# Performance work log

Hardware: AMD Instinct MI355X
Metric: run time of the kernel (lower is better)

## Reference

```python
import jax, jax.numpy as jnp
import numpy as np

N_NODES = 50000
N_EDGES = 1000000
HID = 64
L = 3
EPS_MSG = 1e-7   # GENConv message eps
EPS_SM = 1e-16   # PyG scatter-softmax denominator eps
LN_EPS = 1e-5


def layernorm(x, g, b):
    mu = jnp.mean(x, axis=-1, keepdims=True)
    var = jnp.var(x, axis=-1, keepdims=True)
    return (x - mu) * jax.lax.rsqrt(var + LN_EPS) * g + b


def genconv(x, src, dst, edge_attr, t, W1, b1, g1, be1, W2, b2):
    # message: relu(x_j + e_ij) + eps  -> [E, HID]
    msg = jax.nn.relu(x[src] + edge_attr) + EPS_MSG
    # softmax aggregation over incoming edges of each dst node
    logits = msg * t
    m = jax.ops.segment_max(logits, dst, num_segments=N_NODES)
    m = jnp.where(jnp.isfinite(m), m, 0.0)
    e = jnp.exp(logits - m[dst])
    s = jax.ops.segment_sum(e, dst, num_segments=N_NODES) + EPS_SM
    agg = jax.ops.segment_sum((e / s[dst]) * msg, dst, num_segments=N_NODES)
    # root residual + MLP [64 -> 128 -> 64]
    h = agg + x
    h = h @ W1 + b1
    h = jax.nn.relu(layernorm(h, g1, be1))
    return h @ W2 + b2


def setup_inputs() -> dict:
    key = jax.random.key(0)
    ks = jax.random.split(key, 10)
    inp = {
        'x': jax.random.normal(ks[0], (N_NODES, 16), jnp.float32),
        'edge_attr': jax.random.uniform(ks[1], (N_EDGES, 1), jnp.float32),
        'edge_index': jax.random.randint(ks[2], (2, N_EDGES), 0, N_NODES, jnp.int32),
        'W_node': jax.random.normal(ks[3], (16, HID), jnp.float32) / np.sqrt(16.0),
        'b_node': jnp.zeros((HID,), jnp.float32),
        'W_edge': jax.random.normal(ks[4], (1, HID), jnp.float32),
        'b_edge': jnp.zeros((HID,), jnp.float32),
        't': jnp.ones((L,), jnp.float32),
        'W1': jax.random.normal(ks[5], (L, HID, 2 * HID), jnp.float32) / np.sqrt(float(HID)),
        'b1': jnp.zeros((L, 2 * HID), jnp.float32),
        'ln_g': jnp.ones((L, 2 * HID), jnp.float32),
        'ln_b': jnp.zeros((L, 2 * HID), jnp.float32),
        'W2': jax.random.normal(ks[6], (L, 2 * HID, HID), jnp.float32) / np.sqrt(2.0 * HID),
        'b2': jnp.zeros((L, HID), jnp.float32),
        'norm_g': jnp.ones((L, HID), jnp.float32),
        'norm_b': jnp.zeros((L, HID), jnp.float32),
        'W_lin': jax.random.normal(ks[7], (HID, 64), jnp.float32) / np.sqrt(float(HID)),
        'b_lin': jnp.zeros((64,), jnp.float32),
    }
    return inp


def reference(x, edge_attr, edge_index, W_node, b_node, W_edge, b_edge, t,
              W1, b1, ln_g, ln_b, W2, b2, norm_g, norm_b, W_lin, b_lin):
    src, dst = edge_index[0], edge_index[1]
    h = x @ W_node + b_node                 # [N, HID]
    ea = edge_attr @ W_edge + b_edge        # [E, HID]
    # layer 0: conv only
    h = genconv(h, src, dst, ea, t[0], W1[0], b1[0], ln_g[0], ln_b[0], W2[0], b2[0])
    # layers 1..L-1: res+ blocks (norm -> relu -> conv -> residual); dropout is identity in eval
    for i in range(1, L):
        z = jax.nn.relu(layernorm(h, norm_g[i], norm_b[i]))
        h = h + genconv(z, src, dst, ea, t[i], W1[i], b1[i], ln_g[i], ln_b[i], W2[i], b2[i])
    # final norm/act reuses layer 0's norm
    h = jax.nn.relu(layernorm(h, norm_g[0], norm_b[0]))
    # adaptive avg/max pool (N, 64) -> (1, 32): pool over all nodes, channel bins of 2
    avg = h.mean(axis=0).reshape(32, 2).mean(axis=1)
    mx = h.max(axis=0).reshape(32, 2).max(axis=1)
    emb = jnp.concatenate([avg, mx])[None, :]   # [1, 64]
    return emb @ W_lin + b_lin                  # [1, 64]
```

## Files before the change

### kernel.cpp

```cpp
#include <hip/hip_runtime.h>
#include <math.h>

#define N_NODES 50000
#define N_EDGES 1000000
#define HID 64
#define CAP 64
#define N_TILES (N_NODES / 16)
#define NB_MLP 512
#define VB_S 72
#define UB_S 136
#define NB_ENC ((N_NODES + 3) / 4)
#define NB_WPREP ((3 * 8192 + 255) / 256)
#define NBK 196
#define BKCAP 6144
#define EPB 4096
#define NB1 ((N_EDGES + EPB - 1) / EPB)
static_assert(N_NODES % 16 == 0, "tile math");
static_assert(N_NODES <= 65536, "src must fit in 16 bits");

typedef __attribute__((ext_vector_type(8))) short short8;
typedef __attribute__((ext_vector_type(4))) float f32x4;

__device__ __forceinline__ unsigned short f2bf(float x) {
    unsigned u = __float_as_uint(x);
    u += 0x7FFFu + ((u >> 16) & 1u);
    return (unsigned short)(u >> 16);
}
__device__ __forceinline__ float bfbits_hi(unsigned pk) {
    return __uint_as_float(pk & 0xFFFF0000u);
}
__device__ __forceinline__ float bf2f(unsigned short v) {
    return __uint_as_float(((unsigned)v) << 16);
}
__device__ __forceinline__ unsigned addpk(unsigned a, unsigned b) {
    float lo = __uint_as_float(a << 16) + __uint_as_float(b << 16);
    float hi = __uint_as_float(a & 0xFFFF0000u) + __uint_as_float(b & 0xFFFF0000u);
    return (unsigned)f2bf(lo) | ((unsigned)f2bf(hi) << 16);
}

__global__ __launch_bounds__(256) void k_front(
    const float* __restrict__ x, const float* __restrict__ Wn,
    const float* __restrict__ bn, unsigned short* __restrict__ zb,
    const float* __restrict__ W1, const float* __restrict__ W2,
    unsigned short* __restrict__ w1p, unsigned short* __restrict__ w2p) {
    int b = blockIdx.x;
    if (b < NB_ENC) {
        int n = b * 4 + (threadIdx.x >> 6);
        int c = threadIdx.x & 63;
        if (n >= N_NODES) return;
        float acc = bn[c];
        const float* xr = x + n * 16;
        #pragma unroll
        for (int k = 0; k < 16; ++k) acc = fmaf(xr[k], Wn[k * 64 + c], acc);
        zb[n * 64 + c] = f2bf(acc);
    } else {
        int i = (b - NB_ENC) * 256 + threadIdx.x;
        if (i >= 3 * 8192) return;
        int L = i >> 13, r = i & 8191;
        int j = r & 7, lane = (r >> 3) & 63;
        int quad = lane >> 4, col = lane & 15;
        {
            int st = r >> 9;
            int s = st >> 3, t = st & 7;
            w1p[i] = f2bf(W1[L * 8192 + (s * 32 + quad * 8 + j) * 128 + t * 16 + col]);
        }
        {
            int ft = r >> 9;
            int s = ft >> 2, t = ft & 3;
            w2p[i] = f2bf(W2[L * 8192 + (s * 32 + quad * 8 + j) * 64 + t * 16 + col]);
        }
    }
}

__global__ __launch_bounds__(256) void k_bin1(
    const int* __restrict__ ei, const float* __restrict__ eattr,
    int* __restrict__ gcnt, uint2* __restrict__ coarse) {
    __shared__ unsigned pk_l[EPB];
    __shared__ unsigned short dst_l[EPB];
    __shared__ unsigned spk[EPB];
    __shared__ unsigned short sdst[EPB];
    __shared__ int hist[NBK], loc[NBK], gbase[NBK], cur[NBK];
    __shared__ int inc[256];
    int tid = threadIdx.x;
    int e0 = blockIdx.x * EPB;
    int nel = N_EDGES - e0; if (nel > EPB) nel = EPB;
    for (int b = tid; b < NBK; b += 256) { hist[b] = 0; cur[b] = 0; }
    __syncthreads();
    for (int j = tid; j < nel; j += 256) {
        int i = e0 + j;
        int d = ei[N_EDGES + i];
        unsigned pk = ((unsigned)f2bf(eattr[i]) << 16) | (unsigned)(ei[i] & 0xFFFF);
        pk_l[j] = pk; dst_l[j] = (unsigned short)d;
        atomicAdd(&hist[d >> 8], 1);
    }
    __syncthreads();
    int v = (tid < NBK) ? hist[tid] : 0;
    inc[tid] = v;
    __syncthreads();
    #pragma unroll
    for (int dd = 1; dd < 256; dd <<= 1) {
        int t2 = (tid >= dd) ? inc[tid - dd] : 0;
        __syncthreads();
        inc[tid] += t2;
        __syncthreads();
    }
    if (tid < NBK) {
        loc[tid] = inc[tid] - v;
        gbase[tid] = atomicAdd(&gcnt[tid], v);
    }
    __syncthreads();
    for (int j = tid; j < nel; j += 256) {
        int bkt = dst_l[j] >> 8;
        int r = atomicAdd(&cur[bkt], 1);
        int pos = loc[bkt] + r;
        spk[pos] = pk_l[j]; sdst[pos] = dst_l[j];
    }
    __syncthreads();
    for (int j = tid; j < nel; j += 256) {
        int d = sdst[j];
        int bkt = d >> 8;
        int off = gbase[bkt] + (j - loc[bkt]);
        if (off < BKCAP) coarse[(size_t)bkt * BKCAP + off] = make_uint2(spk[j], (unsigned)d);
    }
}

__global__ __launch_bounds__(256) void k_bin2(
    const int* __restrict__ gcnt, const uint2* __restrict__ coarse,
    int* __restrict__ cnt, unsigned int* __restrict__ s_pack) {
    __shared__ unsigned epk[BKCAP];
    __shared__ unsigned char eln[BKCAP];
    __shared__ unsigned spk[BKCAP];
    __shared__ unsigned char sln[BKCAP];
    __shared__ int hist[256], cur[256], inc2[256];
    int tid = threadIdx.x;
    int b = blockIdx.x;
    int m = gcnt[b]; if (m > BKCAP) m = BKCAP;
    hist[tid] = 0; cur[tid] = 0;
    __syncthreads();
    for (int j = tid; j < m; j += 256) {
        uint2 e = coarse[(size_t)b * BKCAP + j];
        epk[j] = e.x;
        int ln = (int)(e.y & 255u);
        eln[j] = (unsigned char)ln;
        atomicAdd(&hist[ln], 1);
    }
    __syncthreads();
    int v = hist[tid];
    inc2[tid] = v;
    __syncthreads();
    #pragma unroll
    for (int dd = 1; dd < 256; dd <<= 1) {
        int t2 = (tid >= dd) ? inc2[tid - dd] : 0;
        __syncthreads();
        inc2[tid] += t2;
        __syncthreads();
    }
    int lv = inc2[tid] - v;
    __syncthreads();
    hist[tid] = lv;
    int node = b * 256 + tid;
    if (node < N_NODES) cnt[node] = v;
    __syncthreads();
    for (int j = tid; j < m; j += 256) {
        int ln = eln[j];
        int r = atomicAdd(&cur[ln], 1);
        int pos = hist[ln] + r;
        spk[pos] = epk[j]; sln[pos] = (unsigned char)ln;
    }
    __syncthreads();
    for (int j = tid; j < m; j += 256) {
        int ln = sln[j];
        int k = j - hist[ln];
        if (k < CAP) s_pack[(size_t)(b * 256 + ln) * CAP + k] = spk[j];
    }
}

__global__ __launch_bounds__(256) void k_agg(
    const unsigned short* __restrict__ zb, const int* __restrict__ cnt,
    const unsigned int* __restrict__ s_pack,
    const float* __restrict__ We, const float* __restrict__ be,
    const float* __restrict__ t, int layer, unsigned short* __restrict__ aggb) {
    int wid = (blockIdx.x * blockDim.x + threadIdx.x) >> 6;
    int lane = threadIdx.x & 63;
    if (wid >= N_NODES) return;
    int deg = cnt[wid];
    deg = (deg < CAP) ? deg : CAP;
    int beg = wid * CAP, end = beg + deg;
    int half = lane >> 5;
    int c2 = lane & 31;
    float we0 = We[2 * c2], we1 = We[2 * c2 + 1];
    float bv0 = be[2 * c2], bv1 = be[2 * c2 + 1];
    float tl = t[layer];
    const unsigned* zbu = (const unsigned*)zb;
    float s0 = 0.f, s1 = 0.f, n0 = 0.f, n1 = 0.f;
    int i = beg;
    for (; i + 7 < end; i += 8) {
        unsigned pk[4];
        #pragma unroll
        for (int j = 0; j < 4; ++j) {
            unsigned pa = s_pack[i + 2 * j];
            unsigned pb = s_pack[i + 2 * j + 1];
            pk[j] = half ? pb : pa;
        }
        unsigned zu[4];
        #pragma unroll
        for (int j = 0; j < 4; ++j) zu[j] = zbu[(pk[j] & 0xFFFFu) * 32 + c2];
        #pragma unroll
        for (int j = 0; j < 4; ++j) {
            float ea = bfbits_hi(pk[j]);
            float z0 = __uint_as_float(zu[j] << 16);
            float z1 = __uint_as_float(zu[j] & 0xFFFF0000u);
            float m0 = fmaxf(z0 + fmaf(ea, we0, bv0), 0.f) + 1e-7f;
            float m1 = fmaxf(z1 + fmaf(ea, we1, bv1), 0.f) + 1e-7f;
            float p0 = __expf(m0 * tl), p1 = __expf(m1 * tl);
            s0 += p0; n0 = fmaf(p0, m0, n0);
            s1 += p1; n1 = fmaf(p1, m1, n1);
        }
    }
    for (; i + 1 < end; i += 2) {
        unsigned pa = s_pack[i], pb = s_pack[i + 1];
        unsigned pk = half ? pb : pa;
        unsigned zu = zbu[(pk & 0xFFFFu) * 32 + c2];
        float ea = bfbits_hi(pk);
        float z0 = __uint_as_float(zu << 16);
        float z1 = __uint_as_float(zu & 0xFFFF0000u);
        float m0 = fmaxf(z0 + fmaf(ea, we0, bv0), 0.f) + 1e-7f;
        float m1 = fmaxf(z1 + fmaf(ea, we1, bv1), 0.f) + 1e-7f;
        float p0 = __expf(m0 * tl), p1 = __expf(m1 * tl);
        s0 += p0; n0 = fmaf(p0, m0, n0);
        s1 += p1; n1 = fmaf(p1, m1, n1);
    }
    if (i < end) {
        unsigned pk = s_pack[i];
        unsigned zu = zbu[(pk & 0xFFFFu) * 32 + c2];
        float ea = bfbits_hi(pk);
        float z0 = __uint_as_float(zu << 16);
        float z1 = __uint_as_float(zu & 0xFFFF0000u);
        float m0 = fmaxf(z0 + fmaf(ea, we0, bv0), 0.f) + 1e-7f;
        float m1 = fmaxf(z1 + fmaf(ea, we1, bv1), 0.f) + 1e-7f;
        float p0 = __expf(m0 * tl), p1 = __expf(m1 * tl);
        if (half == 0) {
            s0 += p0; n0 = fmaf(p0, m0, n0);
            s1 += p1; n1 = fmaf(p1, m1, n1);
        }
    }
    s0 += __shfl_xor(s0, 32, 64); n0 += __shfl_xor(n0, 32, 64);
    s1 += __shfl_xor(s1, 32, 64); n1 += __shfl_xor(n1, 32, 64);
    if (half == 0) {
        unsigned r = (unsigned)f2bf(n0 / (s0 + 1e-16f)) |
                     ((unsigned)f2bf(n1 / (s1 + 1e-16f)) << 16);
        ((unsigned*)aggb)[wid * 32 + c2] = r;
    }
}

__global__ __launch_bounds__(256) void k_mlp(
    const unsigned short* __restrict__ aggb, unsigned short* __restrict__ zb,
    unsigned short* __restrict__ hb,
    const unsigned short* __restrict__ w1p, const unsigned short* __restrict__ w2p,
    const float* __restrict__ b1,
    const float* __restrict__ g1, const float* __restrict__ be1,
    const float* __restrict__ b2,
    const float* __restrict__ ng, const float* __restrict__ nb, int mode,
    float* __restrict__ pb_sum, float* __restrict__ pb_max) {
    __shared__ unsigned short w1s[8192];
    __shared__ unsigned short w2s[8192];
    __shared__ unsigned short vbuf[4][16 * VB_S];
    __shared__ unsigned short ubuf[4][16 * UB_S];
    __shared__ float lssum[4][4][16], lsmax[4][4][16];
    int lane = threadIdx.x & 63;
    int wave = threadIdx.x >> 6;
    int col = lane & 15, quad = lane >> 4;
    unsigned short* vb = vbuf[wave];
    unsigned short* ub = ubuf[wave];

    {
        const uint4* s1 = (const uint4*)w1p;
        const uint4* s2 = (const uint4*)w2p;
        uint4* d1 = (uint4*)w1s;
        uint4* d2 = (uint4*)w2s;
        #pragma unroll
        for (int i = 0; i < 4; ++i) {
            d1[threadIdx.x + i * 256] = s1[threadIdx.x + i * 256];
            d2[threadIdx.x + i * 256] = s2[threadIdx.x + i * 256];
        }
    }
    __syncthreads();

    float b1f[8], g1f[8], e1f[8];
    #pragma unroll
    for (int t = 0; t < 8; ++t) {
        int ch = t * 16 + col;
        b1f[t] = b1[ch]; g1f[t] = g1[ch]; e1f[t] = be1[ch];
    }
    float b2f_[4], ngf[4], nbf[4];
    #pragma unroll
    for (int t = 0; t < 4; ++t) {
        b2f_[t] = b2[t * 16 + col];
        ngf[t] = ng[t * 16 + col];
        nbf[t] = nb[t * 16 + col];
    }

    float psum[4] = {0.f, 0.f, 0.f, 0.f};
    float pmax[4] = {0.f, 0.f, 0.f, 0.f};
    int nd = lane >> 2;
    int cg = (lane & 3) * 16;

    for (int tile = blockIdx.x * 4 + wave; tile < N_TILES; tile += NB_MLP * 4) {
        int n0 = tile * 16;
        const uint4* ap = (const uint4*)(aggb + (size_t)(n0 + nd) * 64 + cg);
        const uint4* zp = (const uint4*)(zb + (size_t)(n0 + nd) * 64 + cg);
        uint4 a0 = ap[0], a1 = ap[1], z0 = zp[0], z1 = zp[1];
        uint4 r0, r1;
        r0.x = addpk(a0.x, z0.x); r0.y = addpk(a0.y, z0.y);
        r0.z = addpk(a0.z, z0.z); r0.w = addpk(a0.w, z0.w);
        r1.x = addpk(a1.x, z1.x); r1.y = addpk(a1.y, z1.y);
        r1.z = addpk(a1.z, z1.z); r1.w = addpk(a1.w, z1.w);
        uint4* vdst = (uint4*)&vb[nd * VB_S + cg];
        vdst[0] = r0;
        vdst[1] = r1;

        short8 af0 = *(const short8*)&vb[col * VB_S + quad * 8];
        short8 af1 = *(const short8*)&vb[col * VB_S + 32 + quad * 8];

        uint4 h0, h1;
        if (mode >= 1) {
            const uint4* hp = (const uint4*)(hb + (size_t)(n0 + nd) * 64 + cg);
            h0 = hp[0]; h1 = hp[1];
        }

        f32x4 au[8];
        #pragma unroll
        for (int t = 0; t < 8; ++t) {
            short8 w0 = *(const short8*)&w1s[((0 * 8 + t) * 64 + lane) * 8];
            short8 w1 = *(const short8*)&w1s[((1 * 8 + t) * 64 + lane) * 8];
            f32x4 c = {0.f, 0.f, 0.f, 0.f};
            c = __builtin_amdgcn_mfma_f32_16x16x32_bf16(af0, w0, c, 0, 0, 0);
            c = __builtin_amdgcn_mfma_f32_16x16x32_bf16(af1, w1, c, 0, 0, 0);
            au[t] = c;
        }
        #pragma unroll
        for (int r = 0; r < 4; ++r) {
            float sx = 0.f, sq = 0.f;
            #pragma unroll
            for (int t = 0; t < 8; ++t) {
                float v = au[t][r] + b1f[t];
                sx += v; sq += v * v;
            }
            #pragma unroll
            for (int mask = 1; mask < 16; mask <<= 1) {
                sx += __shfl_xor(sx, mask, 64);
                sq += __shfl_xor(sq, mask, 64);
            }
            float mu = sx * (1.f / 128.f);
            float var = sq * (1.f / 128.f) - mu * mu;
            float rs = rsqrtf(var + 1e-5f);
            int row = quad * 4 + r;
            #pragma unroll
            for (int t = 0; t < 8; ++t) {
                float v = au[t][r] + b1f[t];
                float y = fmaxf(fmaf((v - mu) * rs, g1f[t], e1f[t]), 0.f);
                ub[row * UB_S + t * 16 + col] = f2bf(y);
            }
        }
        f32x4 oc[4];
        #pragma unroll
        for (int t = 0; t < 4; ++t) oc[t] = (f32x4){0.f, 0.f, 0.f, 0.f};
        #pragma unroll
        for (int s = 0; s < 4; ++s) {
            short8 a = *(const short8*)&ub[col * UB_S + s * 32 + quad * 8];
            #pragma unroll
            for (int t = 0; t < 4; ++t) {
                short8 w = *(const short8*)&w2s[((s * 4 + t) * 64 + lane) * 8];
                oc[t] = __builtin_amdgcn_mfma_f32_16x16x32_bf16(a, w, oc[t], 0, 0, 0);
            }
        }
        if (mode >= 1) {
            uint4* hdst = (uint4*)&vb[nd * VB_S + cg];
            hdst[0] = h0;
            hdst[1] = h1;
        }
        #pragma unroll
        for (int r = 0; r < 4; ++r) {
            int row = quad * 4 + r;
            float val[4];
            #pragma unroll
            for (int t = 0; t < 4; ++t) {
                val[t] = oc[t][r] + b2f_[t];
                if (mode >= 1) val[t] += bf2f(vb[row * VB_S + t * 16 + col]);
            }
            float sx = 0.f, sq = 0.f;
            #pragma unroll
            for (int t = 0; t < 4; ++t) { sx += val[t]; sq += val[t] * val[t]; }
            #pragma unroll
            for (int mask = 1; mask < 16; mask <<= 1) {
                sx += __shfl_xor(sx, mask, 64);
                sq += __shfl_xor(sq, mask, 64);
            }
            float mu = sx * (1.f / 64.f);
            float var = sq * (1.f / 64.f) - mu * mu;
            float rs = rsqrtf(var + 1e-5f);
            #pragma unroll
            for (int t = 0; t < 4; ++t) {
                float y = fmaxf(fmaf((val[t] - mu) * rs, ngf[t], nbf[t]), 0.f);
                if (mode <= 1) {
                    vb[row * VB_S + t * 16 + col] = f2bf(val[t]);
                    ub[row * UB_S + t * 16 + col] = f2bf(y);
                } else {
                    psum[t] += y;
                    pmax[t] = fmaxf(pmax[t], y);
                }
            }
        }
        if (mode <= 1) {
            const uint4* hsrc = (const uint4*)&vb[nd * VB_S + cg];
            const uint4* zsrc = (const uint4*)&ub[nd * UB_S + cg];
            uint4* hdst = (uint4*)(hb + (size_t)(n0 + nd) * 64 + cg);
            uint4* zdst = (uint4*)(zb + (size_t)(n0 + nd) * 64 + cg);
            hdst[0] = hsrc[0]; hdst[1] = hsrc[1];
            zdst[0] = zsrc[0]; zdst[1] = zsrc[1];
        }
    }
    if (mode == 2) {
        #pragma unroll
        for (int t = 0; t < 4; ++t) {
            psum[t] += __shfl_xor(psum[t], 16, 64);
            psum[t] += __shfl_xor(psum[t], 32, 64);
            pmax[t] = fmaxf(pmax[t], __shfl_xor(pmax[t], 16, 64));
            pmax[t] = fmaxf(pmax[t], __shfl_xor(pmax[t], 32, 64));
        }
        if (quad == 0) {
            #pragma unroll
            for (int t = 0; t < 4; ++t) {
                lssum[wave][t][col] = psum[t];
                lsmax[wave][t][col] = pmax[t];
            }
        }
        __syncthreads();
        if (wave == 0) {
            int t = lane >> 4, c = lane & 15;
            float s = lssum[0][t][c] + lssum[1][t][c] + lssum[2][t][c] + lssum[3][t][c];
            float mx = fmaxf(fmaxf(lsmax[0][t][c], lsmax[1][t][c]),
                             fmaxf(lsmax[2][t][c], lsmax[3][t][c]));
            pb_sum[blockIdx.x * 64 + lane] = s;
            pb_max[blockIdx.x * 64 + lane] = mx;
        }
    }
}

__global__ __launch_bounds__(1024) void k_head(
    const float* __restrict__ pb_sum, const float* __restrict__ pb_max,
    const float* __restrict__ Wl, const float* __restrict__ bl, float* __restrict__ out) {
    __shared__ float sa4[16][64], sm4[16][64];
    __shared__ float sa[64], sm[64], emb[64];
    int t = threadIdx.x;
    int ch = t & 63, part = t >> 6;
    float s = 0.f, mx = 0.f;
    for (int b = part; b < NB_MLP; b += 16) {
        s += pb_sum[b * 64 + ch];
        mx = fmaxf(mx, pb_max[b * 64 + ch]);
    }
    sa4[part][ch] = s; sm4[part][ch] = mx;
    __syncthreads();
    if (t < 64) {
        float ss = 0.f, mm = 0.f;
        #pragma unroll
        for (int q = 0; q < 16; ++q) {
            ss += sa4[q][t];
            mm = fmaxf(mm, sm4[q][t]);
        }
        sa[t] = ss; sm[t] = mm;
    }
    __syncthreads();
    if (t < 64) {
        if (t < 32) {
            emb[t] = (sa[2 * t] + sa[2 * t + 1]) * (0.5f / (float)N_NODES);
        } else {
            int i = t - 32;
            emb[t] = fmaxf(sm[2 * i], sm[2 * i + 1]);
        }
    }
    __syncthreads();
    if (t < 64) {
        float acc = bl[t];
        for (int k = 0; k < 64; ++k) acc = fmaf(emb[k], Wl[k * 64 + t], acc);
        out[t] = acc;
    }
}

extern "C" void kernel_launch(void* const* d_in, const int* in_sizes, int n_in,
                              void* d_out, int out_size, void* d_ws, size_t ws_size,
                              hipStream_t stream) {
    const float* x     = (const float*)d_in[0];
    const float* eattr = (const float*)d_in[1];
    const int*   ei    = (const int*)d_in[2];
    const float* Wn    = (const float*)d_in[3];
    const float* bn    = (const float*)d_in[4];
    const float* We    = (const float*)d_in[5];
    const float* be    = (const float*)d_in[6];
    const float* t     = (const float*)d_in[7];
    const float* W1    = (const float*)d_in[8];
    const float* b1    = (const float*)d_in[9];
    const float* lg    = (const float*)d_in[10];
    const float* lb    = (const float*)d_in[11];
    const float* W2    = (const float*)d_in[12];
    const float* b2    = (const float*)d_in[13];
    const float* ng    = (const float*)d_in[14];
    const float* nb    = (const float*)d_in[15];
    const float* Wl    = (const float*)d_in[16];
    const float* bl    = (const float*)d_in[17];
    float* out = (float*)d_out;

    char* p = (char*)d_ws;
    unsigned short* hb   = (unsigned short*)p; p += (size_t)N_NODES * 64 * 2;
    unsigned short* zb   = (unsigned short*)p; p += (size_t)N_NODES * 64 * 2;
    unsigned short* aggb = (unsigned short*)p; p += (size_t)N_NODES * 64 * 2;
    unsigned int* s_pack = (unsigned int*)p; p += (size_t)N_NODES * CAP * 4;
    int* cnt    = (int*)p;  p += (size_t)N_NODES * 4;
    int* gcnt   = (int*)p;  p += (size_t)256 * 4;
    uint2* coarse = (uint2*)p; p += (size_t)NBK * BKCAP * 8;
    float* pb_sum = (float*)p; p += (size_t)NB_MLP * 64 * 4;
    float* pb_max = (float*)p; p += (size_t)NB_MLP * 64 * 4;
    unsigned short* w1p = (unsigned short*)p; p += (size_t)3 * 8192 * 2;
    unsigned short* w2p = (unsigned short*)p; p += (size_t)3 * 8192 * 2;

    hipMemsetAsync(gcnt, 0, (size_t)NBK * sizeof(int), stream);

    k_front<<<NB_ENC + NB_WPREP, 256, 0, stream>>>(x, Wn, bn, zb, W1, W2, w1p, w2p);
    k_bin1<<<NB1, 256, 0, stream>>>(ei, eattr, gcnt, coarse);
    k_bin2<<<NBK, 256, 0, stream>>>(gcnt, coarse, cnt, s_pack);

    k_agg<<<(N_NODES + 3) / 4, 256, 0, stream>>>(zb, cnt, s_pack, We, be, t, 0, aggb);
    k_mlp<<<NB_MLP, 256, 0, stream>>>(aggb, zb, hb, w1p, w2p, b1, lg, lb, b2,
                                      ng + 64, nb + 64, 0, pb_sum, pb_max);
    k_agg<<<(N_NODES + 3) / 4, 256, 0, stream>>>(zb, cnt, s_pack, We, be, t, 1, aggb);
    k_mlp<<<NB_MLP, 256, 0, stream>>>(aggb, zb, hb, w1p + 8192, w2p + 8192,
                                      b1 + 128, lg + 128, lb + 128, b2 + 64,
                                      ng + 128, nb + 128, 1, pb_sum, pb_max);
    k_agg<<<(N_NODES + 3) / 4, 256, 0, stream>>>(zb, cnt, s_pack, We, be, t, 2, aggb);
    k_mlp<<<NB_MLP, 256, 0, stream>>>(aggb, zb, hb, w1p + 2 * 8192, w2p + 2 * 8192,
                                      b1 + 2 * 128, lg + 2 * 128, lb + 2 * 128, b2 + 2 * 64,
                                      ng, nb, 2, pb_sum, pb_max);

    k_head<<<1, 1024, 0, stream>>>(pb_sum, pb_max, Wl, bl, out);
}
```

Before: 297.5 us.

## Fuse aggregation into per-tile MLP kernel and merge binning into front kernel

Removes the separate aggregation kernel: each wave now aggregates its 16-node tile in registers and feeds the MFMA MLP directly, using ping-pong z buffers instead of an agg buffer. The first binning pass is folded into the front kernel, and the second pass is split into two half-bucket blocks for more parallelism. Weights are read from global memory rather than staged in LDS, and the grid is sized to one tile per wave. This cuts launches and the agg buffer round trip, but aggregation parallelism drops from one wave per node to one wave per 16 nodes, and the per-tile gather latency is serialized.

Measured after the change: 475.9 us. +60.0%, slower.

```diff
diff --git a/kernel.cpp b/kernel.cpp
--- a/kernel.cpp
+++ b/kernel.cpp
@@ -6,7 +6,7 @@
 #define HID 64
 #define CAP 64
 #define N_TILES (N_NODES / 16)
-#define NB_MLP 512
+#define NB_MLP 782
 #define VB_S 72
 #define UB_S 136
 #define NB_ENC ((N_NODES + 3) / 4)
@@ -42,10 +42,60 @@
     const float* __restrict__ x, const float* __restrict__ Wn,
     const float* __restrict__ bn, unsigned short* __restrict__ zb,
     const float* __restrict__ W1, const float* __restrict__ W2,
-    unsigned short* __restrict__ w1p, unsigned short* __restrict__ w2p) {
+    unsigned short* __restrict__ w1p, unsigned short* __restrict__ w2p,
+    const int* __restrict__ ei, const float* __restrict__ eattr,
+    int* __restrict__ gcnt, uint2* __restrict__ coarse) {
+    __shared__ unsigned pk_l[EPB];
+    __shared__ unsigned short dst_l[EPB];
+    __shared__ unsigned spk[EPB];
+    __shared__ unsigned short sdst[EPB];
+    __shared__ int hist[NBK], loc[NBK], gbase[NBK], cur[NBK];
+    __shared__ int inc[256];
     int b = blockIdx.x;
-    if (b < NB_ENC) {
-        int n = b * 4 + (threadIdx.x >> 6);
+    if (b < NB1) {
+        int tid = threadIdx.x;
+        int e0 = b * EPB;
+        int nel = N_EDGES - e0; if (nel > EPB) nel = EPB;
+        for (int q = tid; q < NBK; q += 256) { hist[q] = 0; cur[q] = 0; }
+        __syncthreads();
+        for (int j = tid; j < nel; j += 256) {
+            int i = e0 + j;
+            int d = ei[N_EDGES + i];
+            unsigned pk = ((unsigned)f2bf(eattr[i]) << 16) | (unsigned)(ei[i] & 0xFFFF);
+            pk_l[j] = pk; dst_l[j] = (unsigned short)d;
+            atomicAdd(&hist[d >> 8], 1);
+        }
+        __syncthreads();
+        int v = (tid < NBK) ? hist[tid] : 0;
+        inc[tid] = v;
+        __syncthreads();
+        #pragma unroll
+        for (int dd = 1; dd < 256; dd <<= 1) {
+            int t2 = (tid >= dd) ? inc[tid - dd] : 0;
+            __syncthreads();
+            inc[tid] += t2;
+            __syncthreads();
+        }
+        if (tid < NBK) {
+            loc[tid] = inc[tid] - v;
+            gbase[tid] = atomicAdd(&gcnt[tid], v);
+        }
+        __syncthreads();
+        for (int j = tid; j < nel; j += 256) {
+            int bkt = dst_l[j] >> 8;
+            int r = atomicAdd(&cur[bkt], 1);
+            int pos = loc[bkt] + r;
+            spk[pos] = pk_l[j]; sdst[pos] = dst_l[j];
+        }
+        __syncthreads();
+        for (int j = tid; j < nel; j += 256) {
+            int d = sdst[j];
+            int bkt = d >> 8;
+            int off = gbase[bkt] + (j - loc[bkt]);
+            if (off < BKCAP) coarse[(size_t)bkt * BKCAP + off] = make_uint2(spk[j], (unsigned)d);
+        }
+    } else if (b < NB1 + NB_ENC) {
+        int n = (b - NB1) * 4 + (threadIdx.x >> 6);
         int c = threadIdx.x & 63;
         if (n >= N_NODES) return;
         float acc = bn[c];
@@ -54,7 +104,7 @@
         for (int k = 0; k < 16; ++k) acc = fmaf(xr[k], Wn[k * 64 + c], acc);
         zb[n * 64 + c] = f2bf(acc);
     } else {
-        int i = (b - NB_ENC) * 256 + threadIdx.x;
+        int i = (b - NB1 - NB_ENC) * 256 + threadIdx.x;
         if (i >= 3 * 8192) return;
         int L = i >> 13, r = i & 8191;
         int j = r & 7, lane = (r >> 3) & 63;
@@ -72,58 +122,6 @@
     }
 }
 
-__global__ __launch_bounds__(256) void k_bin1(
-    const int* __restrict__ ei, const float* __restrict__ eattr,
-    int* __restrict__ gcnt, uint2* __restrict__ coarse) {
-    __shared__ unsigned pk_l[EPB];
-    __shared__ unsigned short dst_l[EPB];
-    __shared__ unsigned spk[EPB];
-    __shared__ unsigned short sdst[EPB];
-    __shared__ int hist[NBK], loc[NBK], gbase[NBK], cur[NBK];
-    __shared__ int inc[256];
-    int tid = threadIdx.x;
-    int e0 = blockIdx.x * EPB;
-    int nel = N_EDGES - e0; if (nel > EPB) nel = EPB;
-    for (int b = tid; b < NBK; b += 256) { hist[b] = 0; cur[b] = 0; }
-    __syncthreads();
-    for (int j = tid; j < nel; j += 256) {
-        int i = e0 + j;
-        int d = ei[N_EDGES + i];
-        unsigned pk = ((unsigned)f2bf(eattr[i]) << 16) | (unsigned)(ei[i] & 0xFFFF);
-        pk_l[j] = pk; dst_l[j] = (unsigned short)d;
-        atomicAdd(&hist[d >> 8], 1);
-    }
-    __syncthreads();
-    int v = (tid < NBK) ? hist[tid] : 0;
-    inc[tid] = v;
-    __syncthreads();
-    #pragma unroll
-    for (int dd = 1; dd < 256; dd <<= 1) {
-        int t2 = (tid >= dd) ? inc[tid - dd] : 0;
-        __syncthreads();
-        inc[tid] += t2;
-        __syncthreads();
-    }
-    if (tid < NBK) {
-        loc[tid] = inc[tid] - v;
-        gbase[tid] = atomicAdd(&gcnt[tid], v);
-    }
-    __syncthreads();
-    for (int j = tid; j < nel; j += 256) {
-        int bkt = dst_l[j] >> 8;
-        int r = atomicAdd(&cur[bkt], 1);
-        int pos = loc[bkt] + r;
-        spk[pos] = pk_l[j]; sdst[pos] = dst_l[j];
-    }
-    __syncthreads();
-    for (int j = tid; j < nel; j += 256) {
-        int d = sdst[j];
-        int bkt = d >> 8;
-        int off = gbase[bkt] + (j - loc[bkt]);
-        if (off < BKCAP) coarse[(size_t)bkt * BKCAP + off] = make_uint2(spk[j], (unsigned)d);
-    }
-}
-
 __global__ __launch_bounds__(256) void k_bin2(
     const int* __restrict__ gcnt, const uint2* __restrict__ coarse,
     int* __restrict__ cnt, unsigned int* __restrict__ s_pack) {
@@ -131,139 +129,66 @@
     __shared__ unsigned char eln[BKCAP];
     __shared__ unsigned spk[BKCAP];
     __shared__ unsigned char sln[BKCAP];
-    __shared__ int hist[256], cur[256], inc2[256];
+    __shared__ int hist[128], loc[128], cur[128], inc2[128];
     int tid = threadIdx.x;
-    int b = blockIdx.x;
-    int m = gcnt[b]; if (m > BKCAP) m = BKCAP;
-    hist[tid] = 0; cur[tid] = 0;
+    int bkt = blockIdx.x >> 1;
+    int hsel = blockIdx.x & 1;
+    int m = gcnt[bkt]; if (m > BKCAP) m = BKCAP;
+    if (tid < 128) { hist[tid] = 0; cur[tid] = 0; }
     __syncthreads();
     for (int j = tid; j < m; j += 256) {
-        uint2 e = coarse[(size_t)b * BKCAP + j];
+        uint2 e = coarse[(size_t)bkt * BKCAP + j];
         epk[j] = e.x;
         int ln = (int)(e.y & 255u);
         eln[j] = (unsigned char)ln;
-        atomicAdd(&hist[ln], 1);
-    }
-    __syncthreads();
-    int v = hist[tid];
-    inc2[tid] = v;
+        if ((ln >> 7) == hsel) atomicAdd(&hist[ln & 127], 1);
+    }
+    __syncthreads();
+    int v = (tid < 128) ? hist[tid] : 0;
+    if (tid < 128) inc2[tid] = v;
     __syncthreads();
     #pragma unroll
-    for (int dd = 1; dd < 256; dd <<= 1) {
-        int t2 = (tid >= dd) ? inc2[tid - dd] : 0;
-        __syncthreads();
-        inc2[tid] += t2;
-        __syncthreads();
-    }
-    int lv = inc2[tid] - v;
-    __syncthreads();
-    hist[tid] = lv;
-    int node = b * 256 + tid;
-    if (node < N_NODES) cnt[node] = v;
-    __syncthreads();
+    for (int dd = 1; dd < 128; dd <<= 1) {
+        int t2 = (tid >= dd && tid < 128) ? inc2[tid - dd] : 0;
+        __syncthreads();
+        if (tid < 128) inc2[tid] += t2;
+        __syncthreads();
+    }
+    if (tid < 128) {
+        loc[tid] = inc2[tid] - v;
+        int node = bkt * 256 + hsel * 128 + tid;
+        if (node < N_NODES) cnt[node] = v;
+    }
+    __syncthreads();
+    int mh = inc2[127];
     for (int j = tid; j < m; j += 256) {
         int ln = eln[j];
-        int r = atomicAdd(&cur[ln], 1);
-        int pos = hist[ln] + r;
-        spk[pos] = epk[j]; sln[pos] = (unsigned char)ln;
-    }
-    __syncthreads();
-    for (int j = tid; j < m; j += 256) {
+        if ((ln >> 7) == hsel) {
+            int r = atomicAdd(&cur[ln & 127], 1);
+            int pos = loc[ln & 127] + r;
+            spk[pos] = epk[j]; sln[pos] = (unsigned char)ln;
+        }
+    }
+    __syncthreads();
+    for (int j = tid; j < mh; j += 256) {
         int ln = sln[j];
-        int k = j - hist[ln];
-        if (k < CAP) s_pack[(size_t)(b * 256 + ln) * CAP + k] = spk[j];
-    }
-}
-
-__global__ __launch_bounds__(256) void k_agg(
-    const unsigned short* __restrict__ zb, const int* __restrict__ cnt,
-    const unsigned int* __restrict__ s_pack,
+        int k = j - loc[ln & 127];
+        if (k < CAP) s_pack[(size_t)(bkt * 256 + ln) * CAP + k] = spk[j];
+    }
+}
+
+__global__ __launch_bounds__(256) void k_layer(
+    const unsigned short* __restrict__ zin, unsigned short* __restrict__ zout,
+    unsigned short* __restrict__ hb,
+    const int* __restrict__ cnt, const unsigned int* __restrict__ s_pack,
     const float* __restrict__ We, const float* __restrict__ be,
-    const float* __restrict__ t, int layer, unsigned short* __restrict__ aggb) {
-    int wid = (blockIdx.x * blockDim.x + threadIdx.x) >> 6;
-    int lane = threadIdx.x & 63;
-    if (wid >= N_NODES) return;
-    int deg = cnt[wid];
-    deg = (deg < CAP) ? deg : CAP;
-    int beg = wid * CAP, end = beg + deg;
-    int half = lane >> 5;
-    int c2 = lane & 31;
-    float we0 = We[2 * c2], we1 = We[2 * c2 + 1];
-    float bv0 = be[2 * c2], bv1 = be[2 * c2 + 1];
-    float tl = t[layer];
-    const unsigned* zbu = (const unsigned*)zb;
-    float s0 = 0.f, s1 = 0.f, n0 = 0.f, n1 = 0.f;
-    int i = beg;
-    for (; i + 7 < end; i += 8) {
-        unsigned pk[4];
-        #pragma unroll
-        for (int j = 0; j < 4; ++j) {
-            unsigned pa = s_pack[i + 2 * j];
-            unsigned pb = s_pack[i + 2 * j + 1];
-            pk[j] = half ? pb : pa;
-        }
-        unsigned zu[4];
-        #pragma unroll
-        for (int j = 0; j < 4; ++j) zu[j] = zbu[(pk[j] & 0xFFFFu) * 32 + c2];
-        #pragma unroll
-        for (int j = 0; j < 4; ++j) {
-            float ea = bfbits_hi(pk[j]);
-            float z0 = __uint_as_float(zu[j] << 16);
-            float z1 = __uint_as_float(zu[j] & 0xFFFF0000u);
-            float m0 = fmaxf(z0 + fmaf(ea, we0, bv0), 0.f) + 1e-7f;
-            float m1 = fmaxf(z1 + fmaf(ea, we1, bv1), 0.f) + 1e-7f;
-            float p0 = __expf(m0 * tl), p1 = __expf(m1 * tl);
-            s0 += p0; n0 = fmaf(p0, m0, n0);
-            s1 += p1; n1 = fmaf(p1, m1, n1);
-        }
-    }
-    for (; i + 1 < end; i += 2) {
-        unsigned pa = s_pack[i], pb = s_pack[i + 1];
-        unsigned pk = half ? pb : pa;
-        unsigned zu = zbu[(pk & 0xFFFFu) * 32 + c2];
-        float ea = bfbits_hi(pk);
-        float z0 = __uint_as_float(zu << 16);
-        float z1 = __uint_as_float(zu & 0xFFFF0000u);
-        float m0 = fmaxf(z0 + fmaf(ea, we0, bv0), 0.f) + 1e-7f;
-        float m1 = fmaxf(z1 + fmaf(ea, we1, bv1), 0.f) + 1e-7f;
-        float p0 = __expf(m0 * tl), p1 = __expf(m1 * tl);
-        s0 += p0; n0 = fmaf(p0, m0, n0);
-        s1 += p1; n1 = fmaf(p1, m1, n1);
-    }
-    if (i < end) {
-        unsigned pk = s_pack[i];
-        unsigned zu = zbu[(pk & 0xFFFFu) * 32 + c2];
-        float ea = bfbits_hi(pk);
-        float z0 = __uint_as_float(zu << 16);
-        float z1 = __uint_as_float(zu & 0xFFFF0000u);
-        float m0 = fmaxf(z0 + fmaf(ea, we0, bv0), 0.f) + 1e-7f;
-        float m1 = fmaxf(z1 + fmaf(ea, we1, bv1), 0.f) + 1e-7f;
-        float p0 = __expf(m0 * tl), p1 = __expf(m1 * tl);
-        if (half == 0) {
-            s0 += p0; n0 = fmaf(p0, m0, n0);
-            s1 += p1; n1 = fmaf(p1, m1, n1);
-        }
-    }
-    s0 += __shfl_xor(s0, 32, 64); n0 += __shfl_xor(n0, 32, 64);
-    s1 += __shfl_xor(s1, 32, 64); n1 += __shfl_xor(n1, 32, 64);
-    if (half == 0) {
-        unsigned r = (unsigned)f2bf(n0 / (s0 + 1e-16f)) |
-                     ((unsigned)f2bf(n1 / (s1 + 1e-16f)) << 16);
-        ((unsigned*)aggb)[wid * 32 + c2] = r;
-    }
-}
-
-__global__ __launch_bounds__(256) void k_mlp(
-    const unsigned short* __restrict__ aggb, unsigned short* __restrict__ zb,
-    unsigned short* __restrict__ hb,
+    const float* __restrict__ t, int layer,
     const unsigned short* __restrict__ w1p, const unsigned short* __restrict__ w2p,
     const float* __restrict__ b1,
     const float* __restrict__ g1, const float* __restrict__ be1,
     const float* __restrict__ b2,
     const float* __restrict__ ng, const float* __restrict__ nb, int mode,
     float* __restrict__ pb_sum, float* __restrict__ pb_max) {
-    __shared__ unsigned short w1s[8192];
-    __shared__ unsigned short w2s[8192];
     __shared__ unsigned short vbuf[4][16 * VB_S];
     __shared__ unsigned short ubuf[4][16 * UB_S];
     __shared__ float lssum[4][4][16], lsmax[4][4][16];
@@ -272,53 +197,99 @@
     int col = lane & 15, quad = lane >> 4;
     unsigned short* vb = vbuf[wave];
     unsigned short* ub = ubuf[wave];
-
-    {
-        const uint4* s1 = (const uint4*)w1p;
-        const uint4* s2 = (const uint4*)w2p;
-        uint4* d1 = (uint4*)w1s;
-        uint4* d2 = (uint4*)w2s;
-        #pragma unroll
-        for (int i = 0; i < 4; ++i) {
-            d1[threadIdx.x + i * 256] = s1[threadIdx.x + i * 256];
-            d2[threadIdx.x + i * 256] = s2[threadIdx.x + i * 256];
-        }
-    }
-    __syncthreads();
-
-    float b1f[8], g1f[8], e1f[8];
-    #pragma unroll
-    for (int t = 0; t < 8; ++t) {
-        int ch = t * 16 + col;
-        b1f[t] = b1[ch]; g1f[t] = g1[ch]; e1f[t] = be1[ch];
-    }
-    float b2f_[4], ngf[4], nbf[4];
-    #pragma unroll
-    for (int t = 0; t < 4; ++t) {
-        b2f_[t] = b2[t * 16 + col];
-        ngf[t] = ng[t * 16 + col];
-        nbf[t] = nb[t * 16 + col];
-    }
-
+    int tile = blockIdx.x * 4 + wave;
     float psum[4] = {0.f, 0.f, 0.f, 0.f};
     float pmax[4] = {0.f, 0.f, 0.f, 0.f};
-    int nd = lane >> 2;
-    int cg = (lane & 3) * 16;
-
-    for (int tile = blockIdx.x * 4 + wave; tile < N_TILES; tile += NB_MLP * 4) {
+
+    if (tile < N_TILES) {
         int n0 = tile * 16;
-        const uint4* ap = (const uint4*)(aggb + (size_t)(n0 + nd) * 64 + cg);
-        const uint4* zp = (const uint4*)(zb + (size_t)(n0 + nd) * 64 + cg);
-        uint4 a0 = ap[0], a1 = ap[1], z0 = zp[0], z1 = zp[1];
-        uint4 r0, r1;
-        r0.x = addpk(a0.x, z0.x); r0.y = addpk(a0.y, z0.y);
-        r0.z = addpk(a0.z, z0.z); r0.w = addpk(a0.w, z0.w);
-        r1.x = addpk(a1.x, z1.x); r1.y = addpk(a1.y, z1.y);
-        r1.z = addpk(a1.z, z1.z); r1.w = addpk(a1.w, z1.w);
+        {
+            int half = lane >> 5;
+            int c2 = lane & 31;
+            float we0 = We[2 * c2], we1 = We[2 * c2 + 1];
+            float bv0 = be[2 * c2], bv1 = be[2 * c2 + 1];
+            float tl = t[layer];
+            const unsigned* zbu = (const unsigned*)zin;
+            for (int ln = 0; ln < 16; ++ln) {
+                int wid = n0 + ln;
+                int deg = cnt[wid];
+                deg = (deg < CAP) ? deg : CAP;
+                int beg = wid * CAP, end = beg + deg;
+                float s0 = 0.f, s1 = 0.f, nn0 = 0.f, nn1 = 0.f;
+                int i = beg;
+                for (; i + 7 < end; i += 8) {
+                    unsigned pk[4];
+                    #pragma unroll
+                    for (int j = 0; j < 4; ++j) {
+                        unsigned pa = s_pack[i + 2 * j];
+                        unsigned pb = s_pack[i + 2 * j + 1];
+                        pk[j] = half ? pb : pa;
+                    }
+                    unsigned zu[4];
+                    #pragma unroll
+                    for (int j = 0; j < 4; ++j) zu[j] = zbu[(pk[j] & 0xFFFFu) * 32 + c2];
+                    #pragma unroll
+                    for (int j = 0; j < 4; ++j) {
+                        float ea = bfbits_hi(pk[j]);
+                        float z0 = __uint_as_float(zu[j] << 16);
+                        float z1 = __uint_as_float(zu[j] & 0xFFFF0000u);
+                        float m0 = fmaxf(z0 + fmaf(ea, we0, bv0), 0.f) + 1e-7f;
+                        float m1 = fmaxf(z1 + fmaf(ea, we1, bv1), 0.f) + 1e-7f;
+                        float p0 = __expf(m0 * tl), p1 = __expf(m1 * tl);
+                        s0 += p0; nn0 = fmaf(p0, m0, nn0);
+                        s1 += p1; nn1 = fmaf(p1, m1, nn1);
+                    }
+                }
+                for (; i + 1 < end; i += 2) {
+                    unsigned pa = s_pack[i], pb = s_pack[i + 1];
+                    unsigned pk = half ? pb : pa;
+                    unsigned zu = zbu[(pk & 0xFFFFu) * 32 + c2];
+                    float ea = bfbits_hi(pk);
+                    float z0 = __uint_as_float(zu << 16);
+                    float z1 = __uint_as_float(zu & 0xFFFF0000u);
+                    float m0 = fmaxf(z0 + fmaf(ea, we0, bv0), 0.f) + 1e-7f;
+                    float m1 = fmaxf(z1 + fmaf(ea, we1, bv1), 0.f) + 1e-7f;
+                    float p0 = __expf(m0 * tl), p1 = __expf(m1 * tl);
+                    s0 += p0; nn0 = fmaf(p0, m0, nn0);
+                    s1 += p1; nn1 = fmaf(p1, m1, nn1);
+                }
+                if (i < end) {
+                    unsigned pk = s_pack[i];
+                    unsigned zu = zbu[(pk & 0xFFFFu) * 32 + c2];
+                    float ea = bfbits_hi(pk);
+                    float z0 = __uint_as_float(zu << 16);
+                    float z1 = __uint_as_float(zu & 0xFFFF0000u);
+                    float m0 = fmaxf(z0 + fmaf(ea, we0, bv0), 0.f) + 1e-7f;
+                    float m1 = fmaxf(z1 + fmaf(ea, we1, bv1), 0.f) + 1e-7f;
+                    float p0 = __expf(m0 * tl), p1 = __expf(m1 * tl);
+                    if (half == 0) {
+                        s0 += p0; nn0 = fmaf(p0, m0, nn0);
+                        s1 += p1; nn1 = fmaf(p1, m1, nn1);
+                    }
+                }
+                s0 += __shfl_xor(s0, 32, 64); nn0 += __shfl_xor(nn0, 32, 64);
+                s1 += __shfl_xor(s1, 32, 64); nn1 += __shfl_xor(nn1, 32, 64);
+                if (half == 0) {
+                    unsigned r = (unsigned)f2bf(nn0 / (s0 + 1e-16f)) |
+                                 ((unsigned)f2bf(nn1 / (s1 + 1e-16f)) << 16);
+                    *(unsigned*)&vb[ln * VB_S + 2 * c2] = r;
+                }
+            }
+        }
+        int nd = lane >> 2;
+        int cg = (lane & 3) * 16;
         uint4* vdst = (uint4*)&vb[nd * VB_S + cg];
-        vdst[0] = r0;
-        vdst[1] = r1;
-
+        {
+            const uint4* zp = (const uint4*)(zin + (size_t)(n0 + nd) * 64 + cg);
+            uint4 z0 = zp[0], z1 = zp[1];
+            uint4 a0 = vdst[0], a1 = vdst[1];
+            uint4 r0, r1;
+            r0.x = addpk(a0.x, z0.x); r0.y = addpk(a0.y, z0.y);
+            r0.z = addpk(a0.z, z0.z); r0.w = addpk(a0.w, z0.w);
+            r1.x = addpk(a1.x, z1.x); r1.y = addpk(a1.y, z1.y);
+            r1.z = addpk(a1.z, z1.z); r1.w = addpk(a1.w, z1.w);
+            vdst[0] = r0; vdst[1] = r1;
+        }
         short8 af0 = *(const short8*)&vb[col * VB_S + quad * 8];
         short8 af1 = *(const short8*)&vb[col * VB_S + 32 + quad * 8];
 
@@ -328,22 +299,36 @@
             h0 = hp[0]; h1 = hp[1];
         }
 
+        float b1f[8], g1f[8], e1f[8];
+        #pragma unroll
+        for (int tt = 0; tt < 8; ++tt) {
+            int ch = tt * 16 + col;
+            b1f[tt] = b1[ch]; g1f[tt] = g1[ch]; e1f[tt] = be1[ch];
+        }
+        float b2f_[4], ngf[4], nbf[4];
+        #pragma unroll
+        for (int tt = 0; tt < 4; ++tt) {
+            b2f_[tt] = b2[tt * 16 + col];
+            ngf[tt] = ng[tt * 16 + col];
+            nbf[tt] = nb[tt * 16 + col];
+        }
+
         f32x4 au[8];
         #pragma unroll
-        for (int t = 0; t < 8; ++t) {
-            short8 w0 = *(const short8*)&w1s[((0 * 8 + t) * 64 + lane) * 8];
-            short8 w1 = *(const short8*)&w1s[((1 * 8 + t) * 64 + lane) * 8];
+        for (int tt = 0; tt < 8; ++tt) {
+            short8 w0 = *(const short8*)&w1p[((0 * 8 + tt) * 64 + lane) * 8];
+            short8 w1 = *(const short8*)&w1p[((1 * 8 + tt) * 64 + lane) * 8];
             f32x4 c = {0.f, 0.f, 0.f, 0.f};
             c = __builtin_amdgcn_mfma_f32_16x16x32_bf16(af0, w0, c, 0, 0, 0);
             c = __builtin_amdgcn_mfma_f32_16x16x32_bf16(af1, w1, c, 0, 0, 0);
-            au[t] = c;
+            au[tt] = c;
         }
         #pragma unroll
         for (int r = 0; r < 4; ++r) {
             float sx = 0.f, sq = 0.f;
             #pragma unroll
-            for (int t = 0; t < 8; ++t) {
-                float v = au[t][r] + b1f[t];
+            for (int tt = 0; tt < 8; ++tt) {
+                float v = au[tt][r] + b1f[tt];
                 sx += v; sq += v * v;
             }
             #pragma unroll
@@ -356,41 +341,39 @@
             float rs = rsqrtf(var + 1e-5f);
             int row = quad * 4 + r;
             #pragma unroll
-            for (int t = 0; t < 8; ++t) {
-                float v = au[t][r] + b1f[t];
-                float y = fmaxf(fmaf((v - mu) * rs, g1f[t], e1f[t]), 0.f);
-                ub[row * UB_S + t * 16 + col] = f2bf(y);
+            for (int tt = 0; tt < 8; ++tt) {
+                float v = au[tt][r] + b1f[tt];
+                float y = fmaxf(fmaf((v - mu) * rs, g1f[tt], e1f[tt]), 0.f);
+                ub[row * UB_S + tt * 16 + col] = f2bf(y);
             }
         }
         f32x4 oc[4];
         #pragma unroll
-        for (int t = 0; t < 4; ++t) oc[t] = (f32x4){0.f, 0.f, 0.f, 0.f};
+        for (int tt = 0; tt < 4; ++tt) oc[tt] = (f32x4){0.f, 0.f, 0.f, 0.f};
         #pragma unroll
         for (int s = 0; s < 4; ++s) {
             short8 a = *(const short8*)&ub[col * UB_S + s * 32 + quad * 8];
             #pragma unroll
-            for (int t = 0; t < 4; ++t) {
-                short8 w = *(const short8*)&w2s[((s * 4 + t) * 64 + lane) * 8];
-                oc[t] = __builtin_amdgcn_mfma_f32_16x16x32_bf16(a, w, oc[t], 0, 0, 0);
+            for (int tt = 0; tt < 4; ++tt) {
+                short8 w = *(const short8*)&w2p[((s * 4 + tt) * 64 + lane) * 8];
+                oc[tt] = __builtin_amdgcn_mfma_f32_16x16x32_bf16(a, w, oc[tt], 0, 0, 0);
             }
         }
         if (mode >= 1) {
-            uint4* hdst = (uint4*)&vb[nd * VB_S + cg];
-            hdst[0] = h0;
-            hdst[1] = h1;
+            vdst[0] = h0; vdst[1] = h1;
         }
         #pragma unroll
         for (int r = 0; r < 4; ++r) {
             int row = quad * 4 + r;
             float val[4];
             #pragma unroll
-            for (int t = 0; t < 4; ++t) {
-                val[t] = oc[t][r] + b2f_[t];
-                if (mode >= 1) val[t] += bf2f(vb[row * VB_S + t * 16 + col]);
+            for (int tt = 0; tt < 4; ++tt) {
+                val[tt] = oc[tt][r] + b2f_[tt];
+                if (mode >= 1) val[tt] += bf2f(vb[row * VB_S + tt * 16 + col]);
             }
             float sx = 0.f, sq = 0.f;
             #pragma unroll
-            for (int t = 0; t < 4; ++t) { sx += val[t]; sq += val[t] * val[t]; }
+            for (int tt = 0; tt < 4; ++tt) { sx += val[tt]; sq += val[tt] * val[tt]; }
             #pragma unroll
             for (int mask = 1; mask < 16; mask <<= 1) {
                 sx += __shfl_xor(sx, mask, 64);
@@ -400,14 +383,14 @@
             float var = sq * (1.f / 64.f) - mu * mu;
             float rs = rsqrtf(var + 1e-5f);
             #pragma unroll
-            for (int t = 0; t < 4; ++t) {
-                float y = fmaxf(fmaf((val[t] - mu) * rs, ngf[t], nbf[t]), 0.f);
+            for (int tt = 0; tt < 4; ++tt) {
+                float y = fmaxf(fmaf((val[tt] - mu) * rs, ngf[tt], nbf[tt]), 0.f);
                 if (mode <= 1) {
-                    vb[row * VB_S + t * 16 + col] = f2bf(val[t]);
-                    ub[row * UB_S + t * 16 + col] = f2bf(y);
+                    vb[row * VB_S + tt * 16 + col] = f2bf(val[tt]);
+                    ub[row * UB_S + tt * 16 + col] = f2bf(y);
                 } else {
-                    psum[t] += y;
-                    pmax[t] = fmaxf(pmax[t], y);
+                    psum[tt] += y;
+                    pmax[tt] = fmaxf(pmax[tt], y);
                 }
             }
         }
@@ -415,32 +398,32 @@
             const uint4* hsrc = (const uint4*)&vb[nd * VB_S + cg];
             const uint4* zsrc = (const uint4*)&ub[nd * UB_S + cg];
             uint4* hdst = (uint4*)(hb + (size_t)(n0 + nd) * 64 + cg);
-            uint4* zdst = (uint4*)(zb + (size_t)(n0 + nd) * 64 + cg);
+            uint4* zdst = (uint4*)(zout + (size_t)(n0 + nd) * 64 + cg);
             hdst[0] = hsrc[0]; hdst[1] = hsrc[1];
             zdst[0] = zsrc[0]; zdst[1] = zsrc[1];
         }
     }
     if (mode == 2) {
         #pragma unroll
-        for (int t = 0; t < 4; ++t) {
-            psum[t] += __shfl_xor(psum[t], 16, 64);
-            psum[t] += __shfl_xor(psum[t], 32, 64);
-            pmax[t] = fmaxf(pmax[t], __shfl_xor(pmax[t], 16, 64));
-            pmax[t] = fmaxf(pmax[t], __shfl_xor(pmax[t], 32, 64));
+        for (int tt = 0; tt < 4; ++tt) {
+            psum[tt] += __shfl_xor(psum[tt], 16, 64);
+            psum[tt] += __shfl_xor(psum[tt], 32, 64);
+            pmax[tt] = fmaxf(pmax[tt], __shfl_xor(pmax[tt], 16, 64));
+            pmax[tt] = fmaxf(pmax[tt], __shfl_xor(pmax[tt], 32, 64));
         }
         if (quad == 0) {
             #pragma unroll
-            for (int t = 0; t < 4; ++t) {
-                lssum[wave][t][col] = psum[t];
-                lsmax[wave][t][col] = pmax[t];
+            for (int tt = 0; tt < 4; ++tt) {
+                lssum[wave][tt][col] = psum[tt];
+                lsmax[wave][tt][col] = pmax[tt];
             }
         }
         __syncthreads();
         if (wave == 0) {
-            int t = lane >> 4, c = lane & 15;
-            float s = lssum[0][t][c] + lssum[1][t][c] + lssum[2][t][c] + lssum[3][t][c];
-            float mx = fmaxf(fmaxf(lsmax[0][t][c], lsmax[1][t][c]),
-                             fmaxf(lsmax[2][t][c], lsmax[3][t][c]));
+            int tt = lane >> 4, c = lane & 15;
+            float s = lssum[0][tt][c] + lssum[1][tt][c] + lssum[2][tt][c] + lssum[3][tt][c];
+            float mx = fmaxf(fmaxf(lsmax[0][tt][c], lsmax[1][tt][c]),
+                             fmaxf(lsmax[2][tt][c], lsmax[3][tt][c]));
             pb_sum[blockIdx.x * 64 + lane] = s;
             pb_max[blockIdx.x * 64 + lane] = mx;
         }
@@ -511,9 +494,9 @@
     float* out = (float*)d_out;
 
     char* p = (char*)d_ws;
-    unsigned short* hb   = (unsigned short*)p; p += (size_t)N_NODES * 64 * 2;
-    unsigned short* zb   = (unsigned short*)p; p += (size_t)N_NODES * 64 * 2;
-    unsigned short* aggb = (unsigned short*)p; p += (size_t)N_NODES * 64 * 2;
+    unsigned short* hb = (unsigned short*)p; p += (size_t)N_NODES * 64 * 2;
+    unsigned short* zA = (unsigned short*)p; p += (size_t)N_NODES * 64 * 2;
+    unsigned short* zB = (unsigned short*)p; p += (size_t)N_NODES * 64 * 2;
     unsigned int* s_pack = (unsigned int*)p; p += (size_t)N_NODES * CAP * 4;
     int* cnt    = (int*)p;  p += (size_t)N_NODES * 4;
     int* gcnt   = (int*)p;  p += (size_t)256 * 4;
@@ -525,21 +508,21 @@
 
     hipMemsetAsync(gcnt, 0, (size_t)NBK * sizeof(int), stream);
 
-    k_front<<<NB_ENC + NB_WPREP, 256, 0, stream>>>(x, Wn, bn, zb, W1, W2, w1p, w2p);
-    k_bin1<<<NB1, 256, 0, stream>>>(ei, eattr, gcnt, coarse);
-    k_bin2<<<NBK, 256, 0, stream>>>(gcnt, coarse, cnt, s_pack);
-
-    k_agg<<<(N_NODES + 3) / 4, 256, 0, stream>>>(zb, cnt, s_pack, We, be, t, 0, aggb);
-    k_mlp<<<NB_MLP, 256, 0, stream>>>(aggb, zb, hb, w1p, w2p, b1, lg, lb, b2,
-                                      ng + 64, nb + 64, 0, pb_sum, pb_max);
-    k_agg<<<(N_NODES + 3) / 4, 256, 0, stream>>>(zb, cnt, s_pack, We, be, t, 1, aggb);
-    k_mlp<<<NB_MLP, 256, 0, stream>>>(aggb, zb, hb, w1p + 8192, w2p + 8192,
-                                      b1 + 128, lg + 128, lb + 128, b2 + 64,
-                                      ng + 128, nb + 128, 1, pb_sum, pb_max);
-    k_agg<<<(N_NODES + 3) / 4, 256, 0, stream>>>(zb, cnt, s_pack, We, be, t, 2, aggb);
-    k_mlp<<<NB_MLP, 256, 0, stream>>>(aggb, zb, hb, w1p + 2 * 8192, w2p + 2 * 8192,
-                                      b1 + 2 * 128, lg + 2 * 128, lb + 2 * 128, b2 + 2 * 64,
-                                      ng, nb, 2, pb_sum, pb_max);
+    k_front<<<NB1 + NB_ENC + NB_WPREP, 256, 0, stream>>>(
+        x, Wn, bn, zA, W1, W2, w1p, w2p, ei, eattr, gcnt, coarse);
+    k_bin2<<<NBK * 2, 256, 0, stream>>>(gcnt, coarse, cnt, s_pack);
+
+    k_layer<<<NB_MLP, 256, 0, stream>>>(zA, zB, hb, cnt, s_pack, We, be, t, 0,
+                                        w1p, w2p, b1, lg, lb, b2,
+                                        ng + 64, nb + 64, 0, pb_sum, pb_max);
+    k_layer<<<NB_MLP, 256, 0, stream>>>(zB, zA, hb, cnt, s_pack, We, be, t, 1,
+                                        w1p + 8192, w2p + 8192,
+                                        b1 + 128, lg + 128, lb + 128, b2 + 64,
+                                        ng + 128, nb + 128, 1, pb_sum, pb_max);
+    k_layer<<<NB_MLP, 256, 0, stream>>>(zA, zB, hb, cnt, s_pack, We, be, t, 2,
+                                        w1p + 2 * 8192, w2p + 2 * 8192,
+                                        b1 + 2 * 128, lg + 2 * 128, lb + 2 * 128, b2 + 2 * 64,
+                                        ng, nb, 2, pb_sum, pb_max);
 
     k_head<<<1, 1024, 0, stream>>>(pb_sum, pb_max, Wl, bl, out);
 }
```
